# Optimization experiments

Hardware: AMD Instinct MI355X
Metric: run time of the kernel (lower is better)

The kernel has to match this reference:

```python
import jax, jax.numpy as jnp
import numpy as np

D, T, B = 128, 64, 512
EPS = 1e-5


def setup_inputs() -> dict:
    key = jax.random.key(0)
    k1, k2, k3, k4, k5 = jax.random.split(key, 5)
    inp = jax.random.normal(k1, (D, T, B), jnp.float32) * 0.1
    returns_partition = jax.random.normal(k2, (D, T, B), jnp.float32) * 0.01
    target = jax.random.normal(k3, (D,), jnp.float32) * 0.1
    hidden = jnp.zeros((D, 1, B), jnp.float32)  # forward arg (overwritten at t=0)
    # diagonally-dominant weight so the per-row denominators v[j,j] stay away from 0
    W = jnp.eye(D, dtype=jnp.float32) + 0.1 * jax.random.normal(k4, (D, D), jnp.float32)
    b = 0.1 * jax.random.normal(k5, (D,), jnp.float32)
    return {"input": inp, "target": target, "returns_partition": returns_partition,
            "hidden": hidden, "W": W, "b": b}


def _recurrence(h, v, absb, pi_bar):
    # h, pi_bar: [D, B]; v: [D, D] (row-normalized); absb: [D]
    d = h.shape[0]
    vd = jnp.diagonal(v)                                  # v[j, j], torch.matmul(vj, e_j)
    s = v @ (h - pi_bar)                                  # [D, B], s[j] = vj . (h - pi_bar)
    lam_p = (absb[:, None] - s) / vd[:, None]
    lam_m = (-absb[:, None] - s) / vd[:, None]
    delta = (jnp.where(s > absb[:, None], lam_p, 0.0)
             + jnp.where(s < -absb[:, None], lam_m, 0.0))  # [D, B]
    # hidden_new_j = h + delta[j] * e_j  =>  v @ (hidden_new_j - pi_bar) = s + v[:, j] (x) delta[j]
    snew = s[None, :, :] + v.T[:, :, None] * delta[:, None, :]      # [J, D, B]
    inside = (snew < absb[None, :, None] + EPS) & (snew > -absb[None, :, None] - EPS)
    # torch: judge_mat[j] = min over rows; then max over j  == any_j(all_k(...))
    judge_mat = jnp.any(jnp.all(inside, axis=1), axis=0).astype(h.dtype)  # [B]

    # sequential per-coordinate projection (order matters: row j uses updated state)
    def body(ht, j):
        sj = v[j] @ (ht - pi_bar)                          # [B]
        lp = (absb[j] - sj) / v[j, j]
        lm = (-absb[j] - sj) / v[j, j]
        dj = jnp.where(sj > absb[j], lp, 0.0) + jnp.where(sj < -absb[j], lm, 0.0)
        return ht.at[j].add(dj), None
    h_temp, _ = jax.lax.scan(body, h, jnp.arange(d))

    # 10-step bisection between pi_bar (feasible) and (1 - judge_mat) * h
    def bis(carry, _):
        h_in, h_out = carry
        h_m = h_in + (h_out - h_in) * 0.5
        sm = v @ (h_m - pi_bar)
        j = jnp.all((sm <= absb[:, None] + EPS) & (sm >= -absb[:, None] - EPS), axis=0)  # [B]
        return (jnp.where(j, h_m, h_in), jnp.where(j, h_out, h_m)), h_m
    h_out0 = (1.0 - judge_mat) * h
    _, h_ms = jax.lax.scan(bis, (pi_bar, h_out0), None, length=10)
    h_m = h_ms[-1]
    return judge_mat * h_temp + (1.0 - judge_mat) * h_m


def reference(input, target, returns_partition, hidden, W, b):
    d, t, bsz = input.shape
    norm = jnp.linalg.norm(W, axis=1, keepdims=True)
    v = W / jnp.maximum(norm, 1e-12)                      # F.normalize(W, p=2, dim=1)
    absb = jnp.abs(b)
    pi_bar = jnp.broadcast_to(target[:, None], (d, bsz))  # [D, B]

    h0 = input[:, 0, :]                                   # t = 0: hidden := input slice
    rs = jnp.moveaxis(returns_partition[:, :t - 1, :], 1, 0)  # [T-1, D, B]

    def step(h, r):
        adj = h * (1.0 + r) / (1.0 + jnp.sum(h * r, axis=0))
        hn = _recurrence(adj, v, absb, pi_bar)
        return hn, hn

    h_last, hs = jax.lax.scan(step, h0, rs)
    output = jnp.concatenate([h0[:, None, :], jnp.moveaxis(hs, 0, 1)], axis=1)  # [D, T, B]
    return output, h_last[:, None, :]
```

## Files before the change

kernel.cpp:

```cpp
#include <hip/hip_runtime.h>
#include <cstdint>

#define D 128
#define T 64
#define B 512
#define EPSF 1e-5f

__device__ __forceinline__ float lane_bcast(float x, int l) {
    return __int_as_float(__builtin_amdgcn_readlane(__float_as_int(x), l));
}

__global__ __launch_bounds__(64) void prep_kernel(const float* __restrict__ W,
                                                  const float* __restrict__ b,
                                                  float* __restrict__ vT,
                                                  float* __restrict__ vd,
                                                  float* __restrict__ absb) {
    const int i = blockIdx.x;
    const int l = threadIdx.x;
    float w0 = W[i * D + l];
    float w1 = W[i * D + l + 64];
    float p = w0 * w0 + w1 * w1;
#pragma unroll
    for (int off = 32; off; off >>= 1) p += __shfl_xor(p, off);
    float norm = sqrtf(p);
    float scale = norm > 1e-12f ? norm : 1e-12f;
    float v0 = w0 / scale;
    float v1 = w1 / scale;
    vT[l * D + i] = v0;
    vT[(l + 64) * D + i] = v1;
    if (i < 64) {
        if (l == i) vd[i] = v0;
    } else {
        if (l == i - 64) vd[i] = v1;
    }
    if (i == 0) {
        absb[l] = fabsf(b[l]);
        absb[l + 64] = fabsf(b[l + 64]);
    }
}

__global__ __launch_bounds__(128, 1) void rnn_kernel(const float* __restrict__ input,
                                                     const float* __restrict__ target,
                                                     const float* __restrict__ returns,
                                                     const float* __restrict__ vTg,
                                                     const float* __restrict__ vdg,
                                                     const float* __restrict__ absbg,
                                                     float* __restrict__ out) {
    __shared__ float vsh[D * D];
    __shared__ __align__(16) float aeps_arr[D];
    __shared__ __align__(16) float sstage[2][D];

    const int tid = threadIdx.x;
    {
        const float4* src = (const float4*)vTg;
        float4* dst = (float4*)vsh;
#pragma unroll
        for (int c = 0; c < 32; ++c) {
            int f = c * 128 + tid;
            int k = f >> 5;
            int i = (f & 31) << 2;
            int ck = (k & 7) << 2;
            int d4 = k * 32 + (((i ^ ck)) >> 2);
            dst[d4] = src[f];
        }
    }
    aeps_arr[tid] = absbg[tid] + EPSF;
    __syncthreads();

    const int w = tid >> 6;
    const int lane = tid & 63;
    const int b = blockIdx.x * 2 + w;
    const int rlo = lane, rhi = lane + 64;

    const float tgt_lo = target[rlo], tgt_hi = target[rhi];
    const float a_lo = absbg[rlo], a_hi = absbg[rhi];
    const float aeps_lo = a_lo + EPSF, aeps_hi = a_hi + EPSF;
    const float vd_lo = vdg[rlo], vd_hi = vdg[rhi];
    const float rvd_lo = 1.0f / vd_lo, rvd_hi = 1.0f / vd_hi;

    int ax[8];
#pragma unroll
    for (int c = 0; c < 8; ++c) ax[c] = rlo ^ (c << 2);

    float vl[D], vh[D];
#pragma unroll
    for (int k = 0; k < D; ++k) {
        int base = k * 128 + ax[k & 7];
        vl[k] = vsh[base];
        vh[k] = vsh[base + 64];
        asm volatile("" : "+a"(vl[k]), "+a"(vh[k]));
    }

    const int cj = (lane & 7) << 2;
    int Abase[8];
#pragma unroll
    for (int c = 0; c < 8; ++c) Abase[c] = lane * 128 + ((c << 2) ^ cj);

    float h_lo = input[rlo * T * B + b];
    float h_hi = input[rhi * T * B + b];
    out[rlo * T * B + b] = h_lo;
    out[rhi * T * B + b] = h_hi;

    float r_lo = returns[rlo * T * B + b];
    float r_hi = returns[rhi * T * B + b];

    for (int t = 1; t < T; ++t) {
        float num_lo = h_lo * (1.0f + r_lo);
        float num_hi = h_hi * (1.0f + r_hi);
        float p = h_lo * r_lo + h_hi * r_hi;
#pragma unroll
        for (int off = 32; off; off >>= 1) p += __shfl_xor(p, off);
        float den = 1.0f + p;
        float adj_lo = num_lo / den;
        float adj_hi = num_hi / den;

        if (t < T - 1) {
            r_lo = returns[rlo * T * B + t * B + b];
            r_hi = returns[rhi * T * B + t * B + b];
        }

        const float x_lo = adj_lo - tgt_lo;
        const float x_hi = adj_hi - tgt_hi;

        float s_lo = 0.0f, s_hi = 0.0f;
#pragma unroll
        for (int k = 0; k < 64; ++k) {
            float xb = lane_bcast(x_lo, k);
            s_lo = fmaf(vl[k], xb, s_lo);
            s_hi = fmaf(vh[k], xb, s_hi);
        }
#pragma unroll
        for (int k = 0; k < 64; ++k) {
            float xb = lane_bcast(x_hi, k);
            s_lo = fmaf(vl[64 + k], xb, s_lo);
            s_hi = fmaf(vh[64 + k], xb, s_hi);
        }

        h_lo = adj_lo;
        h_hi = adj_hi;

        bool viol_lo = (s_lo > a_lo) || (s_lo < -a_lo);
        bool viol_hi = (s_hi > a_hi) || (s_hi < -a_hi);
        uint64_t mlo = __ballot(viol_lo);
        uint64_t mhi = __ballot(viol_hi);

        if ((mlo | mhi) != 0ull) {
            sstage[w][rlo] = s_lo;
            sstage[w][rhi] = s_hi;

            float dl = 0.0f, dh = 0.0f;
            if (s_lo > a_lo) dl = (a_lo - s_lo) / vd_lo;
            else if (s_lo < -a_lo) dl = (-a_lo - s_lo) / vd_lo;
            if (s_hi > a_hi) dh = (a_hi - s_hi) / vd_hi;
            else if (s_hi < -a_hi) dh = (-a_hi - s_hi) / vd_hi;

            int V = __popcll(mlo) + __popcll(mhi);
            bool judge;

            if (V <= 8) {
                bool in_lo = (s_lo < aeps_lo) && (s_lo > -aeps_lo);
                bool in_hi = (s_hi < aeps_hi) && (s_hi > -aeps_hi);
                judge = (__ballot(in_lo && in_hi) == ~0ull);
                if (!judge) {
                    uint64_t t_mlo = mlo, t_mhi = mhi;
                    while (t_mlo | t_mhi) {
                        int j;
                        float dj;
                        if (t_mlo) {
                            int jl = (int)__ffsll((unsigned long long)t_mlo) - 1;
                            t_mlo &= t_mlo - 1;
                            j = jl;
                            dj = lane_bcast(dl, jl);
                        } else {
                            int jh = (int)__ffsll((unsigned long long)t_mhi) - 1;
                            t_mhi &= t_mhi - 1;
                            j = 64 + jh;
                            dj = lane_bcast(dh, jh);
                        }
                        int cjj = (j & 7) << 2;
                        int base = j * 128 + (rlo ^ cjj);
                        float n_lo = fmaf(vsh[base], dj, s_lo);
                        float n_hi = fmaf(vsh[base + 64], dj, s_hi);
                        bool pl = (n_lo < aeps_lo) && (n_lo > -aeps_lo);
                        bool ph = (n_hi < aeps_hi) && (n_hi > -aeps_hi);
                        if (__ballot(pl && ph) == ~0ull) { judge = true; break; }
                    }
                }
            } else {
                float m1 = -1.0f, m2 = -1.0f;
                bool dead = false;
#pragma unroll
                for (int a = 0; a < 4; ++a) {
                    if (!dead) {
#pragma unroll
                        for (int c = 0; c < 8; ++c) {
                            const int i0 = a * 32 + c * 4;
                            const float* p1 = &vsh[Abase[c] + 32 * a];
                            float4 c1 = *(const float4*)p1;
                            float4 c2 = *(const float4*)(p1 + 8192);
                            float4 s4 = *(const float4*)&sstage[w][i0];
                            float4 ae4 = *(const float4*)&aeps_arr[i0];
#pragma unroll
                            for (int e = 0; e < 4; ++e) {
                                float sv = ((const float*)&s4)[e];
                                float ae = ((const float*)&ae4)[e];
                                float f1 = ((const float*)&c1)[e];
                                float f2 = ((const float*)&c2)[e];
                                m1 = fmaxf(m1, fabsf(fmaf(f1, dl, sv)) - ae);
                                m2 = fmaxf(m2, fabsf(fmaf(f2, dh, sv)) - ae);
                            }
                        }
                        if (a < 3) {
                            if ((__ballot(m1 < 0.0f) | __ballot(m2 < 0.0f)) == 0ull)
                                dead = true;
                        }
                    }
                }
                judge = ((__ballot(m1 < 0.0f) | __ballot(m2 < 0.0f)) != 0ull);
            }

            if (judge) {
                uint64_t rem_lo = ~0ull, rem_hi = ~0ull;
                while (true) {
                    uint64_t m1b = __ballot((s_lo > a_lo) || (s_lo < -a_lo)) & rem_lo;
                    uint64_t m2b = __ballot((s_hi > a_hi) || (s_hi < -a_hi)) & rem_hi;
                    int j;
                    if (m1b) {
                        int jl = (int)__ffsll((unsigned long long)m1b) - 1;
                        j = jl;
                        rem_lo = (jl == 63) ? 0ull : (~0ull << (jl + 1));
                    } else if (m2b) {
                        int jh = (int)__ffsll((unsigned long long)m2b) - 1;
                        j = 64 + jh;
                        rem_lo = 0ull;
                        rem_hi = (jh == 63) ? 0ull : (~0ull << (jh + 1));
                    } else {
                        break;
                    }
                    float dl2 = (s_lo > a_lo) ? (a_lo - s_lo) * rvd_lo
                               : ((s_lo < -a_lo) ? (-a_lo - s_lo) * rvd_lo : 0.0f);
                    float dh2 = (s_hi > a_hi) ? (a_hi - s_hi) * rvd_hi
                               : ((s_hi < -a_hi) ? (-a_hi - s_hi) * rvd_hi : 0.0f);
                    float srcv = (j < 64) ? dl2 : dh2;
                    float dj = lane_bcast(srcv, j & 63);
                    if (lane == (j & 63)) {
                        if (j < 64) h_lo += dj; else h_hi += dj;
                    }
                    int cjj = (j & 7) << 2;
                    int base = j * 128 + (rlo ^ cjj);
                    s_lo = fmaf(vsh[base], dj, s_lo);
                    s_hi = fmaf(vsh[base + 64], dj, s_hi);
                }
            } else {
                float hin_lo = tgt_lo, hin_hi = tgt_hi;
                float sin_lo = 0.0f, sin_hi = 0.0f;
                float hout_lo = h_lo, hout_hi = h_hi;
                float sout_lo = s_lo, sout_hi = s_hi;
                float hm_lo = 0.0f, hm_hi = 0.0f;
#pragma unroll
                for (int it = 0; it < 10; ++it) {
                    hm_lo = hin_lo + (hout_lo - hin_lo) * 0.5f;
                    hm_hi = hin_hi + (hout_hi - hin_hi) * 0.5f;
                    float sm_lo = sin_lo + (sout_lo - sin_lo) * 0.5f;
                    float sm_hi = sin_hi + (sout_hi - sin_hi) * 0.5f;
                    bool pl = (sm_lo <= aeps_lo) && (sm_lo >= -aeps_lo);
                    bool ph = (sm_hi <= aeps_hi) && (sm_hi >= -aeps_hi);
                    bool inside = (__ballot(pl && ph) == ~0ull);
                    if (inside) {
                        hin_lo = hm_lo; hin_hi = hm_hi;
                        sin_lo = sm_lo; sin_hi = sm_hi;
                    } else {
                        hout_lo = hm_lo; hout_hi = hm_hi;
                        sout_lo = sm_lo; sout_hi = sm_hi;
                    }
                }
                h_lo = hm_lo;
                h_hi = hm_hi;
            }
        }

        out[rlo * T * B + t * B + b] = h_lo;
        out[rhi * T * B + t * B + b] = h_hi;
    }

    out[D * T * B + rlo * B + b] = h_lo;
    out[D * T * B + rhi * B + b] = h_hi;
}

extern "C" void kernel_launch(void* const* d_in, const int* in_sizes, int n_in,
                              void* d_out, int out_size, void* d_ws, size_t ws_size,
                              hipStream_t stream) {
    const float* input   = (const float*)d_in[0];
    const float* target  = (const float*)d_in[1];
    const float* returns = (const float*)d_in[2];
    const float* W = (const float*)d_in[4];
    const float* b = (const float*)d_in[5];
    float* out = (float*)d_out;

    float* vT   = (float*)d_ws;
    float* vd   = vT + D * D;
    float* absb = vd + D;

    prep_kernel<<<D, 64, 0, stream>>>(W, b, vT, vd, absb);
    rnn_kernel<<<B / 2, 128, 0, stream>>>(input, target, returns, vT, vd, absb, out);
}
```

Baseline: 216.4 us.

## Prefetch next projection column speculatively and simplify judge pre-check

```diff
diff --git a/kernel.cpp b/kernel.cpp
--- a/kernel.cpp
+++ b/kernel.cpp
@@ -47,6 +47,7 @@
                                                      const float* __restrict__ absbg,
                                                      float* __restrict__ out) {
     __shared__ float vsh[D * D];
+    __shared__ __align__(16) float2 vpair[D * 64];
     __shared__ __align__(16) float aeps_arr[D];
     __shared__ __align__(16) float sstage[2][D];
 
@@ -64,6 +65,18 @@
             dst[d4] = src[f];
         }
     }
+#pragma unroll
+    for (int c = 0; c < 32; ++c) {
+        int f = c * 128 + tid;
+        int k = f >> 5;
+        int i0 = (f & 31) << 1;
+        float4 val;
+        val.x = vTg[k * D + i0];
+        val.y = vTg[k * D + i0 + 64];
+        val.z = vTg[k * D + i0 + 1];
+        val.w = vTg[k * D + i0 + 65];
+        *(float4*)&vpair[(k << 6) + (i0 ^ ((k & 3) << 2))] = val;
+    }
     aeps_arr[tid] = absbg[tid] + EPSF;
     __syncthreads();
 
@@ -96,6 +109,7 @@
 #pragma unroll
     for (int c = 0; c < 8; ++c) Abase[c] = lane * 128 + ((c << 2) ^ cj);
 
+
     float h_lo = input[rlo * T * B + b];
     float h_hi = input[rhi * T * B + b];
     out[rlo * T * B + b] = h_lo;
@@ -145,6 +159,10 @@
         uint64_t mhi = __ballot(viol_hi);
 
         if ((mlo | mhi) != 0ull) {
+            int j0 = mlo ? (int)__ffsll((unsigned long long)mlo) - 1
+                         : 64 + (int)__ffsll((unsigned long long)mhi) - 1;
+            float2 p0 = vpair[(j0 << 6) + (lane ^ ((j0 & 3) << 2))];
+
             sstage[w][rlo] = s_lo;
             sstage[w][rhi] = s_hi;
 
@@ -154,39 +172,14 @@
             if (s_hi > a_hi) dh = (a_hi - s_hi) / vd_hi;
             else if (s_hi < -a_hi) dh = (-a_hi - s_hi) / vd_hi;
 
-            int V = __popcll(mlo) + __popcll(mhi);
             bool judge;
 
-            if (V <= 8) {
-                bool in_lo = (s_lo < aeps_lo) && (s_lo > -aeps_lo);
-                bool in_hi = (s_hi < aeps_hi) && (s_hi > -aeps_hi);
-                judge = (__ballot(in_lo && in_hi) == ~0ull);
-                if (!judge) {
-                    uint64_t t_mlo = mlo, t_mhi = mhi;
-                    while (t_mlo | t_mhi) {
-                        int j;
-                        float dj;
-                        if (t_mlo) {
-                            int jl = (int)__ffsll((unsigned long long)t_mlo) - 1;
-                            t_mlo &= t_mlo - 1;
-                            j = jl;
-                            dj = lane_bcast(dl, jl);
-                        } else {
-                            int jh = (int)__ffsll((unsigned long long)t_mhi) - 1;
-                            t_mhi &= t_mhi - 1;
-                            j = 64 + jh;
-                            dj = lane_bcast(dh, jh);
-                        }
-                        int cjj = (j & 7) << 2;
-                        int base = j * 128 + (rlo ^ cjj);
-                        float n_lo = fmaf(vsh[base], dj, s_lo);
-                        float n_hi = fmaf(vsh[base + 64], dj, s_hi);
-                        bool pl = (n_lo < aeps_lo) && (n_lo > -aeps_lo);
-                        bool ph = (n_hi < aeps_hi) && (n_hi > -aeps_hi);
-                        if (__ballot(pl && ph) == ~0ull) { judge = true; break; }
-                    }
-                }
-            } else {
+            bool allviol = (mlo == ~0ull) && (mhi == ~0ull);
+            bool in_lo = (s_lo < aeps_lo) && (s_lo > -aeps_lo);
+            bool in_hi = (s_hi < aeps_hi) && (s_hi > -aeps_hi);
+            judge = !allviol && (__ballot(in_lo && in_hi) == ~0ull);
+
+            if (!judge) {
                 float m1 = -1.0f, m2 = -1.0f;
                 bool dead = false;
 #pragma unroll
@@ -221,35 +214,50 @@
 
             if (judge) {
                 uint64_t rem_lo = ~0ull, rem_hi = ~0ull;
-                while (true) {
-                    uint64_t m1b = __ballot((s_lo > a_lo) || (s_lo < -a_lo)) & rem_lo;
-                    uint64_t m2b = __ballot((s_hi > a_hi) || (s_hi < -a_hi)) & rem_hi;
-                    int j;
-                    if (m1b) {
-                        int jl = (int)__ffsll((unsigned long long)m1b) - 1;
-                        j = jl;
-                        rem_lo = (jl == 63) ? 0ull : (~0ull << (jl + 1));
-                    } else if (m2b) {
-                        int jh = (int)__ffsll((unsigned long long)m2b) - 1;
-                        j = 64 + jh;
-                        rem_lo = 0ull;
-                        rem_hi = (jh == 63) ? 0ull : (~0ull << (jh + 1));
+                uint64_t m1b = mlo, m2b = mhi;
+                int jcur = j0;
+                float2 pcur = p0;
+                while (jcur >= 0) {
+                    uint64_t t1 = m1b, t2 = m2b;
+                    if (jcur < 64) {
+                        t1 &= (jcur == 63) ? 0ull : (~0ull << (jcur + 1));
                     } else {
-                        break;
-                    }
+                        t1 = 0ull;
+                        t2 &= (jcur == 127) ? 0ull : (~0ull << (jcur - 63));
+                    }
+                    int jspec = t1 ? (int)__ffsll((unsigned long long)t1) - 1
+                              : (t2 ? 64 + (int)__ffsll((unsigned long long)t2) - 1 : -1);
+                    float2 pspec;
+                    pspec.x = 0.0f; pspec.y = 0.0f;
+                    if (jspec >= 0)
+                        pspec = vpair[(jspec << 6) + (lane ^ ((jspec & 3) << 2))];
+
                     float dl2 = (s_lo > a_lo) ? (a_lo - s_lo) * rvd_lo
                                : ((s_lo < -a_lo) ? (-a_lo - s_lo) * rvd_lo : 0.0f);
                     float dh2 = (s_hi > a_hi) ? (a_hi - s_hi) * rvd_hi
                                : ((s_hi < -a_hi) ? (-a_hi - s_hi) * rvd_hi : 0.0f);
-                    float srcv = (j < 64) ? dl2 : dh2;
-                    float dj = lane_bcast(srcv, j & 63);
-                    if (lane == (j & 63)) {
-                        if (j < 64) h_lo += dj; else h_hi += dj;
-                    }
-                    int cjj = (j & 7) << 2;
-                    int base = j * 128 + (rlo ^ cjj);
-                    s_lo = fmaf(vsh[base], dj, s_lo);
-                    s_hi = fmaf(vsh[base + 64], dj, s_hi);
+                    float dj = lane_bcast((jcur < 64) ? dl2 : dh2, jcur & 63);
+                    if (lane == (jcur & 63)) {
+                        if (jcur < 64) h_lo += dj; else h_hi += dj;
+                    }
+                    if (jcur < 64) {
+                        rem_lo = (jcur == 63) ? 0ull : (~0ull << (jcur + 1));
+                    } else {
+                        rem_lo = 0ull;
+                        rem_hi = (jcur == 127) ? 0ull : (~0ull << (jcur - 63));
+                    }
+                    s_lo = fmaf(pcur.x, dj, s_lo);
+                    s_hi = fmaf(pcur.y, dj, s_hi);
+
+                    m1b = __ballot((s_lo > a_lo) || (s_lo < -a_lo)) & rem_lo;
+                    m2b = __ballot((s_hi > a_hi) || (s_hi < -a_hi)) & rem_hi;
+                    int jn = m1b ? (int)__ffsll((unsigned long long)m1b) - 1
+                           : (m2b ? 64 + (int)__ffsll((unsigned long long)m2b) - 1 : -1);
+                    if (jn >= 0) {
+                        if (jn == jspec) pcur = pspec;
+                        else pcur = vpair[(jn << 6) + (lane ^ ((jn & 3) << 2))];
+                    }
+                    jcur = jn;
                 }
             } else {
                 float hin_lo = tgt_lo, hin_hi = tgt_hi;
```

New measurement: 361.3 us. 1.67x slower.
